# Kernel tuning notes

Hardware: AMD Instinct MI355X
Metric: run time of the kernel (lower is better)

Reference implementation:

```python
import jax, jax.numpy as jnp
import numpy as np

NUM_HEADS = 8
T = 8  # hardcoded temporal dim in the original forward
MD = 3  # max_displacement -> 7x7 window
EPS = 1e-12  # F.normalize eps


def l2_normalize(x, axis):
    n = jnp.sqrt(jnp.sum(x * x, axis=axis, keepdims=True))
    return x / jnp.maximum(n, EPS)


def correlation_7x7(q, k):
    # q, k: [B, C, H, W]; FlowNet-style correlation, kernel_size=1, max_disp=3.
    # out[b, u, v, h, w] = sum_c q[b,c,h,w] * k[b,c,h+u-3,w+v-3] (zero padded)
    B, C, H, W = q.shape
    kp = jnp.pad(k, ((0, 0), (0, 0), (MD, MD), (MD, MD)))
    outs = []
    for dy in range(2 * MD + 1):
        for dx in range(2 * MD + 1):
            ks = kp[:, :, dy:dy + H, dx:dx + W]
            outs.append(jnp.sum(q * ks, axis=1))  # [B, H, W]
    corr = jnp.stack(outs, axis=1)  # [B, 49, H, W]
    return corr.reshape(B, 2 * MD + 1, 2 * MD + 1, H, W)


def setup_inputs() -> dict:
    key = jax.random.key(0)
    ks = jax.random.split(key, 6)
    B, N, C = 8, 8192, 256
    hd = C // NUM_HEADS
    std = 0.02
    return {
        "x": jax.random.normal(ks[0], (B, N, C), dtype=jnp.float32),
        "w_qk": jax.random.normal(ks[1], (2 * C, C), dtype=jnp.float32) * std,
        "w_corr": jax.random.normal(ks[2], (hd, 49), dtype=jnp.float32) * std,
        "b_corr": jnp.zeros((hd,), dtype=jnp.float32),
        "w_proj": jax.random.normal(ks[3], (C, C), dtype=jnp.float32) * std,
        "b_proj": jnp.zeros((C,), dtype=jnp.float32),
    }


def reference(x, w_qk, w_corr, b_corr, w_proj, b_proj):
    B, N, C = x.shape
    nh = NUM_HEADS
    hd = C // nh
    H = int(np.sqrt(N // T))
    W = H

    # qk projection (no bias): [B, N, 2C] -> q, k each [B, nh, N, hd]
    qk = jnp.einsum('bnc,dc->bnd', x, w_qk)
    qk = qk.reshape(B, N, 2, nh, hd).transpose(2, 0, 3, 1, 4)
    q, k = qk[0], qk[1]

    # 'b n (t h w) d -> (b n) t d h w'
    q = q.reshape(B * nh, T, H, W, hd).transpose(0, 1, 4, 2, 3)
    k = k.reshape(B * nh, T, H, W, hd).transpose(0, 1, 4, 2, 3)

    # temporal postfix: k[t+1], last frame repeated
    k_post = jnp.concatenate([k[:, 1:], k[:, -1:]], axis=1)

    qp = q.reshape(B * nh * T, hd, H, W)
    kp = k_post.reshape(B * nh * T, hd, H, W)
    qp = l2_normalize(qp, axis=1)
    kp = l2_normalize(kp, axis=1)

    corr = correlation_7x7(qp, kp)  # [(B nh T), 7, 7, H, W]
    # 'b u v h w -> b (h w) (u v)'
    corr = corr.transpose(0, 3, 4, 1, 2).reshape(B * nh * T, H * W, 49)

    v = jnp.einsum('bpk,dk->bpd', corr, w_corr) + b_corr  # [(B nh T), HW, hd]

    # '(b n t) (h w) d -> b n (t h w) d' then 'b h n d -> b n (h d)'
    out = v.reshape(B, nh, T * H * W, hd).transpose(0, 2, 1, 3).reshape(B, N, C)
    out = jnp.einsum('bnc,dc->bnd', out, w_proj) + b_proj
    return out
```

## Files before the change

kernel.cpp:

```cpp
#include <hip/hip_runtime.h>

typedef _Float16 half8 __attribute__((ext_vector_type(8)));
typedef _Float16 half2v __attribute__((ext_vector_type(2)));
typedef float float4v __attribute__((ext_vector_type(4)));

__device__ __forceinline__ float dot2acc(unsigned a, unsigned b, float c) {
#if __has_builtin(__builtin_amdgcn_fdot2)
  return __builtin_amdgcn_fdot2(__builtin_bit_cast(half2v, a), __builtin_bit_cast(half2v, b), c, false);
#else
  half2v ha = __builtin_bit_cast(half2v, a);
  half2v hb = __builtin_bit_cast(half2v, b);
  c += (float)ha[0] * (float)hb[0];
  c += (float)ha[1] * (float)hb[1];
  return c;
#endif
}
__device__ __forceinline__ unsigned hscale(unsigned a, float s) {
  half2v ha = __builtin_bit_cast(half2v, a);
  half2v r;
  r[0] = (_Float16)((float)ha[0] * s);
  r[1] = (_Float16)((float)ha[1] * s);
  return __builtin_bit_cast(unsigned, r);
}
__device__ __forceinline__ void gload_lds16(const void* g, void* l) {
  __builtin_amdgcn_global_load_lds((const __attribute__((address_space(1))) unsigned*)g,
                                   (__attribute__((address_space(3))) unsigned*)l, 16, 0, 0);
}

__global__ void cvt_all(const float4* __restrict__ x, const float4* __restrict__ wqk,
                        const float4* __restrict__ wpj,
                        ushort4* __restrict__ x16, ushort4* __restrict__ wqk16,
                        ushort4* __restrict__ wpj16) {
  int b = blockIdx.x;
  const float4* s;
  ushort4* d;
  int i;
  if (b < 16384) { s = x; d = x16; i = b * 256 + threadIdx.x; }
  else if (b < 16512) { s = wqk; d = wqk16; i = (b - 16384) * 256 + threadIdx.x; }
  else { s = wpj; d = wpj16; i = (b - 16512) * 256 + threadIdx.x; }
  float4 v = s[i];
  _Float16 a = (_Float16)v.x, bb = (_Float16)v.y, c = (_Float16)v.z, e = (_Float16)v.w;
  ushort4 o;
  o.x = __builtin_bit_cast(unsigned short, a);
  o.y = __builtin_bit_cast(unsigned short, bb);
  o.z = __builtin_bit_cast(unsigned short, c);
  o.w = __builtin_bit_cast(unsigned short, e);
  d[i] = o;
}

__global__ __launch_bounds__(256, 2)
void gemm_qk(const _Float16* __restrict__ A, const _Float16* __restrict__ Bw,
             _Float16* __restrict__ qo, _Float16* __restrict__ ko) {
  __shared__ _Float16 Ash[4096];
  __shared__ _Float16 Bsh[4096];
  const int tid = threadIdx.x;
  const int lane = tid & 63, w = tid >> 6;
  const int wm = w >> 1, wn = w & 1;
  const int ml = lane & 15, qd = lane >> 4;
  const int m0 = blockIdx.y * 128, n0 = blockIdx.x * 128;

  float4v acc[4][4];
  float4v z = {0.f, 0.f, 0.f, 0.f};
#pragma unroll
  for (int i = 0; i < 4; ++i)
#pragma unroll
    for (int j = 0; j < 4; ++j) acc[i][j] = z;

  const _Float16* Ap = A + (size_t)m0 * 256;
  const _Float16* Bp = Bw + (size_t)n0 * 256;
  const int gr = w * 64 + lane;
  const int row0 = gr >> 2, kb = gr & 3;

  for (int kt = 0; kt < 8; ++kt) {
    int k0 = kt * 32;
    gload_lds16(Ap + row0 * 256 + k0 + kb * 8, Ash + (size_t)(w * 64) * 8);
    gload_lds16(Ap + (row0 + 64) * 256 + k0 + kb * 8, Ash + (size_t)(256 + w * 64) * 8);
    gload_lds16(Bp + row0 * 256 + k0 + kb * 8, Bsh + (size_t)(w * 64) * 8);
    gload_lds16(Bp + (row0 + 64) * 256 + k0 + kb * 8, Bsh + (size_t)(256 + w * 64) * 8);
    __syncthreads();
    half8 af[4], bf[4];
#pragma unroll
    for (int im = 0; im < 4; ++im) {
      af[im] = *(const half8*)(Ash + (wm * 64 + im * 16 + ml) * 32 + qd * 8);
      bf[im] = *(const half8*)(Bsh + (wn * 64 + im * 16 + ml) * 32 + qd * 8);
    }
#pragma unroll
    for (int im = 0; im < 4; ++im)
#pragma unroll
      for (int in = 0; in < 4; ++in)
        acc[im][in] = __builtin_amdgcn_mfma_f32_16x16x32_f16(af[im], bf[in], acc[im][in], 0, 0, 0);
    __syncthreads();
  }

#pragma unroll
  for (int im = 0; im < 4; ++im) {
    int rowr0 = m0 + wm * 64 + im * 16 + qd * 4;
#pragma unroll
    for (int in = 0; in < 4; ++in) {
      int col = n0 + wn * 64 + in * 16 + ml;
      int s = col >> 8, h = (col >> 5) & 7, j = col & 31;
      _Float16* dst = s ? ko : qo;
#pragma unroll
      for (int r = 0; r < 4; ++r) {
        int rowr = rowr0 + r;
        int b = rowr >> 13, n = rowr & 8191;
        int t = n >> 10, yx = n & 1023;
        int p = b * 64 + h * 8 + t;
        dst[((size_t)p * 1024 + yx) * 32 + j] = (_Float16)acc[im][in][r];
      }
    }
  }
}

__global__ __launch_bounds__(256, 4)
void corr_kernel(const _Float16* __restrict__ q16, const _Float16* __restrict__ k16,
                 const float* __restrict__ wcorr, const float* __restrict__ bcorr,
                 _Float16* __restrict__ outp) {
  __shared__ uint4 smem[2304];
  __shared__ uint4 wcs[256];

  const int tid = threadIdx.x;
  const int bx = blockIdx.x;
  const int p = bx >> 2, tile = bx & 3;
  const int y0 = (tile >> 1) * 16, x0 = (tile & 1) * 16;
  const int b = p >> 6, h = (p >> 3) & 7, t = p & 7;
  const int pk = (t < 7) ? p + 1 : p;
  const int ty = tid >> 4, tx = tid & 15;

  _Float16* wch = (_Float16*)wcs;
  for (int idx = tid; idx < 2048; idx += 256) {
    int d = idx >> 6, kk = idx & 63;
    float v = (kk < 49) ? wcorr[d * 49 + kk] : (kk == 49 ? bcorr[d] : 0.f);
    wch[idx] = (_Float16)v;
  }

  const _Float16* kbase = k16 + (size_t)pk * 32768;
#pragma unroll
  for (int i = 0; i < 8; ++i) {
    int g = tid + i * 256;
    if (g < 1936) {
      int vec = g >> 2, part = g & 3;
      int ky = vec / 22, kx = vec - ky * 22;
      int gy = y0 + ky - 3, gx = x0 + kx - 3;
      uint4 val = make_uint4(0u, 0u, 0u, 0u);
      if (gy >= 0 && gy < 32 && gx >= 0 && gx < 32)
        val = *(const uint4*)(kbase + ((size_t)gy * 32 + gx) * 32 + part * 8);
      int slot = (vec << 2) | (part ^ (vec & 3) ^ ((vec >> 2) & 3));
      smem[slot] = val;
    }
  }
  __syncthreads();

  for (int v = tid; v < 484; v += 256) {
    int base = v << 2;
    int sw = (v & 3) ^ ((v >> 2) & 3);
    uint4 gg[4];
#pragma unroll
    for (int pq = 0; pq < 4; ++pq) gg[pq] = smem[base | (pq ^ sw)];
    float ss = 0.f;
#pragma unroll
    for (int pq = 0; pq < 4; ++pq) {
      const unsigned* u = (const unsigned*)&gg[pq];
#pragma unroll
      for (int e = 0; e < 4; ++e) ss = dot2acc(u[e], u[e], ss);
    }
    float sc = 1.f / fmaxf(sqrtf(ss), 1e-12f);
#pragma unroll
    for (int pq = 0; pq < 4; ++pq) {
      unsigned* u = (unsigned*)&gg[pq];
#pragma unroll
      for (int e = 0; e < 4; ++e) u[e] = hscale(u[e], sc);
      smem[base | (pq ^ sw)] = gg[pq];
    }
  }
  __syncthreads();

  const _Float16* qptr = q16 + (size_t)p * 32768 + ((size_t)(y0 + ty) * 32 + (x0 + tx)) * 32;
  uint4 qv[4];
#pragma unroll
  for (int i = 0; i < 4; ++i) qv[i] = *(const uint4*)(qptr + i * 8);
  unsigned* qu = (unsigned*)qv;
  float qss = 0.f;
#pragma unroll
  for (int e = 0; e < 16; ++e) qss = dot2acc(qu[e], qu[e], qss);
  float qsc = 1.f / fmaxf(sqrtf(qss), 1e-12f);
#pragma unroll
  for (int e = 0; e < 16; ++e) qu[e] = hscale(qu[e], qsc);

  float corr[49];
#pragma unroll
  for (int dy = 0; dy < 7; ++dy) {
#pragma unroll
    for (int dx = 0; dx < 7; ++dx) {
      int vec = (ty + dy) * 22 + (tx + dx);
      int base = vec << 2;
      int sw = (vec & 3) ^ ((vec >> 2) & 3);
      float c = 0.f;
#pragma unroll
      for (int pq = 0; pq < 4; ++pq) {
        uint4 kk = smem[base | (pq ^ sw)];
        const unsigned* ku = (const unsigned*)&kk;
#pragma unroll
        for (int e = 0; e < 4; ++e) c = dot2acc(qu[pq * 4 + e], ku[e], c);
      }
      corr[dy * 7 + dx] = c;
    }
  }
  __syncthreads();

#pragma unroll
  for (int i = 0; i < 8; ++i) {
    uint4 val;
    unsigned* vu = (unsigned*)&val;
#pragma unroll
    for (int e = 0; e < 4; ++e) {
      int idx = i * 8 + e * 2;
      half2v hh;
      hh[0] = (_Float16)(idx < 49 ? corr[idx] : (idx == 49 ? 1.f : 0.f));
      hh[1] = (_Float16)(idx + 1 < 49 ? corr[idx + 1] : (idx + 1 == 49 ? 1.f : 0.f));
      vu[e] = __builtin_bit_cast(unsigned, hh);
    }
    smem[tid * 9 + i] = val;
  }
  __syncthreads();

  _Float16* corrm = (_Float16*)smem;
  const int lane = tid & 63, w = tid >> 6;
  const int ml = lane & 15, qd = lane >> 4;
  float4v vacc[4][2];
  float4v z = {0.f, 0.f, 0.f, 0.f};
#pragma unroll
  for (int im = 0; im < 4; ++im) { vacc[im][0] = z; vacc[im][1] = z; }
#pragma unroll
  for (int ks = 0; ks < 2; ++ks) {
    half8 bfrag[2];
#pragma unroll
    for (int nt = 0; nt < 2; ++nt)
      bfrag[nt] = *(const half8*)(wch + (nt * 16 + ml) * 64 + ks * 32 + qd * 8);
#pragma unroll
    for (int im = 0; im < 4; ++im) {
      half8 afrag = *(const half8*)(corrm + (w * 64 + im * 16 + ml) * 72 + ks * 32 + qd * 8);
#pragma unroll
      for (int nt = 0; nt < 2; ++nt)
        vacc[im][nt] = __builtin_amdgcn_mfma_f32_16x16x32_f16(afrag, bfrag[nt], vacc[im][nt], 0, 0, 0);
    }
  }

#pragma unroll
  for (int im = 0; im < 4; ++im) {
#pragma unroll
    for (int nt = 0; nt < 2; ++nt) {
      int d = nt * 16 + ml;
#pragma unroll
      for (int r = 0; r < 4; ++r) {
        int pos = w * 64 + im * 16 + qd * 4 + r;
        int py = pos >> 4, px = pos & 15;
        int n = t * 1024 + (y0 + py) * 32 + (x0 + px);
        outp[(((size_t)b * 8192 + n) << 8) + h * 32 + d] = (_Float16)vacc[im][nt][r];
      }
    }
  }
}

__global__ __launch_bounds__(256, 2)
void gemm_proj(const _Float16* __restrict__ A, const _Float16* __restrict__ Bw,
               const float* __restrict__ bp, float* __restrict__ out) {
  __shared__ _Float16 Ash[4096];
  __shared__ _Float16 Bsh[4096];
  const int tid = threadIdx.x;
  const int lane = tid & 63, w = tid >> 6;
  const int wm = w >> 1, wn = w & 1;
  const int ml = lane & 15, qd = lane >> 4;
  const int m0 = blockIdx.y * 128, n0 = blockIdx.x * 128;

  float4v acc[4][4];
  float4v z = {0.f, 0.f, 0.f, 0.f};
#pragma unroll
  for (int i = 0; i < 4; ++i)
#pragma unroll
    for (int j = 0; j < 4; ++j) acc[i][j] = z;

  const _Float16* Ap = A + (size_t)m0 * 256;
  const _Float16* Bp = Bw + (size_t)n0 * 256;
  const int gr = w * 64 + lane;
  const int row0 = gr >> 2, kb = gr & 3;

  for (int kt = 0; kt < 8; ++kt) {
    int k0 = kt * 32;
    gload_lds16(Ap + row0 * 256 + k0 + kb * 8, Ash + (size_t)(w * 64) * 8);
    gload_lds16(Ap + (row0 + 64) * 256 + k0 + kb * 8, Ash + (size_t)(256 + w * 64) * 8);
    gload_lds16(Bp + row0 * 256 + k0 + kb * 8, Bsh + (size_t)(w * 64) * 8);
    gload_lds16(Bp + (row0 + 64) * 256 + k0 + kb * 8, Bsh + (size_t)(256 + w * 64) * 8);
    __syncthreads();
    half8 af[4], bf[4];
#pragma unroll
    for (int im = 0; im < 4; ++im) {
      af[im] = *(const half8*)(Ash + (wm * 64 + im * 16 + ml) * 32 + qd * 8);
      bf[im] = *(const half8*)(Bsh + (wn * 64 + im * 16 + ml) * 32 + qd * 8);
    }
#pragma unroll
    for (int im = 0; im < 4; ++im)
#pragma unroll
      for (int in = 0; in < 4; ++in)
        acc[im][in] = __builtin_amdgcn_mfma_f32_16x16x32_f16(af[im], bf[in], acc[im][in], 0, 0, 0);
    __syncthreads();
  }

#pragma unroll
  for (int im = 0; im < 4; ++im) {
    int rowr0 = m0 + wm * 64 + im * 16 + qd * 4;
#pragma unroll
    for (int in = 0; in < 4; ++in) {
      int col = n0 + wn * 64 + in * 16 + ml;
      float bias = bp[col];
#pragma unroll
      for (int r = 0; r < 4; ++r)
        out[(size_t)(rowr0 + r) * 256 + col] = acc[im][in][r] + bias;
    }
  }
}

extern "C" void kernel_launch(void* const* d_in, const int* in_sizes, int n_in,
                              void* d_out, int out_size, void* d_ws, size_t ws_size,
                              hipStream_t stream) {
  const float* x      = (const float*)d_in[0];
  const float* w_qk   = (const float*)d_in[1];
  const float* w_corr = (const float*)d_in[2];
  const float* b_corr = (const float*)d_in[3];
  const float* w_proj = (const float*)d_in[4];
  const float* b_proj = (const float*)d_in[5];
  float* out = (float*)d_out;

  char* ws = (char*)d_ws;
  _Float16* x16   = (_Float16*)(ws);
  _Float16* q16   = (_Float16*)(ws + 33554432);
  _Float16* k16   = (_Float16*)(ws + 67108864);
  _Float16* op16  = (_Float16*)(ws + 100663296);
  _Float16* wqk16 = (_Float16*)(ws + 134217728);
  _Float16* wpj16 = (_Float16*)(ws + 134479872);

  cvt_all<<<16576, 256, 0, stream>>>((const float4*)x, (const float4*)w_qk, (const float4*)w_proj,
                                     (ushort4*)x16, (ushort4*)wqk16, (ushort4*)wpj16);
  gemm_qk<<<dim3(4, 512), 256, 0, stream>>>(x16, wqk16, q16, k16);
  corr_kernel<<<2048, 256, 0, stream>>>(q16, k16, w_corr, b_corr, op16);
  gemm_proj<<<dim3(2, 512), 256, 0, stream>>>(op16, wpj16, b_proj, out);
}
```

Baseline: 235.1 us.

## Compute 7x7 correlation with MFMA tiles instead of scalar dot2 loops

After: 244.1 us. 3.8% more time.

```diff
diff --git a/kernel.cpp b/kernel.cpp
--- a/kernel.cpp
+++ b/kernel.cpp
@@ -112,12 +112,15 @@
   }
 }
 
-__global__ __launch_bounds__(256, 4)
+__global__ __launch_bounds__(256, 2)
 void corr_kernel(const _Float16* __restrict__ q16, const _Float16* __restrict__ k16,
                  const float* __restrict__ wcorr, const float* __restrict__ bcorr,
                  _Float16* __restrict__ outp) {
-  __shared__ uint4 smem[2304];
-  __shared__ uint4 wcs[256];
+  __shared__ __align__(16) _Float16 S[38400];
+  _Float16* kt = S;
+  _Float16* corrh = S + 15488;
+  _Float16* wch = S + 35968;
+  constexpr int DUMP = 22528;
 
   const int tid = threadIdx.x;
   const int bx = blockIdx.x;
@@ -125,9 +128,18 @@
   const int y0 = (tile >> 1) * 16, x0 = (tile & 1) * 16;
   const int b = p >> 6, h = (p >> 3) & 7, t = p & 7;
   const int pk = (t < 7) ? p + 1 : p;
-  const int ty = tid >> 4, tx = tid & 15;
-
-  _Float16* wch = (_Float16*)wcs;
+
+  const int lane = tid & 63, w = tid >> 6;
+  const int ml = lane & 15, qd = lane >> 4;
+
+  const _Float16* qbase = q16 + (size_t)p * 32768;
+  half8 afrag[4];
+#pragma unroll
+  for (int yi = 0; yi < 4; ++yi) {
+    int yy = 4 * w + yi;
+    afrag[yi] = *(const half8*)(qbase + ((size_t)(y0 + yy) * 32 + (x0 + ml)) * 32 + qd * 8);
+  }
+
   for (int idx = tid; idx < 2048; idx += 256) {
     int d = idx >> 6, kk = idx & 63;
     float v = (kk < 49) ? wcorr[d * 49 + kk] : (kk == 49 ? bcorr[d] : 0.f);
@@ -145,90 +157,80 @@
       uint4 val = make_uint4(0u, 0u, 0u, 0u);
       if (gy >= 0 && gy < 32 && gx >= 0 && gx < 32)
         val = *(const uint4*)(kbase + ((size_t)gy * 32 + gx) * 32 + part * 8);
-      int slot = (vec << 2) | (part ^ (vec & 3) ^ ((vec >> 2) & 3));
-      smem[slot] = val;
-    }
-  }
+      *(uint4*)(kt + (size_t)g * 8) = val;
+    }
+  }
+
+#pragma unroll
+  for (int yi = 0; yi < 4; ++yi) {
+    unsigned* au = (unsigned*)&afrag[yi];
+    float ss = 0.f;
+#pragma unroll
+    for (int e = 0; e < 4; ++e) ss = dot2acc(au[e], au[e], ss);
+    ss += __shfl_xor(ss, 16);
+    ss += __shfl_xor(ss, 32);
+    float sc = 1.f / fmaxf(sqrtf(ss), 1e-12f);
+#pragma unroll
+    for (int e = 0; e < 4; ++e) au[e] = hscale(au[e], sc);
+  }
+
+  {
+    uint4 pat = make_uint4(0x3C000000u, 0u, 0u, 0u);
+    uint4 zz = make_uint4(0u, 0u, 0u, 0u);
+    *(uint4*)(corrh + (size_t)tid * 80 + 48) = pat;
+    *(uint4*)(corrh + (size_t)tid * 80 + 56) = zz;
+  }
+
   __syncthreads();
 
-  for (int v = tid; v < 484; v += 256) {
-    int base = v << 2;
-    int sw = (v & 3) ^ ((v >> 2) & 3);
-    uint4 gg[4];
-#pragma unroll
-    for (int pq = 0; pq < 4; ++pq) gg[pq] = smem[base | (pq ^ sw)];
-    float ss = 0.f;
-#pragma unroll
-    for (int pq = 0; pq < 4; ++pq) {
-      const unsigned* u = (const unsigned*)&gg[pq];
+#pragma unroll
+  for (int i = 0; i < 8; ++i) {
+    int g = tid + i * 256;
+    if (g < 1936) {
+      uint4 val = *(const uint4*)(kt + (size_t)g * 8);
+      unsigned* u = (unsigned*)&val;
+      float ss = 0.f;
 #pragma unroll
       for (int e = 0; e < 4; ++e) ss = dot2acc(u[e], u[e], ss);
-    }
-    float sc = 1.f / fmaxf(sqrtf(ss), 1e-12f);
-#pragma unroll
-    for (int pq = 0; pq < 4; ++pq) {
-      unsigned* u = (unsigned*)&gg[pq];
+      ss += __shfl_xor(ss, 1);
+      ss += __shfl_xor(ss, 2);
+      float sc = 1.f / fmaxf(sqrtf(ss), 1e-12f);
 #pragma unroll
       for (int e = 0; e < 4; ++e) u[e] = hscale(u[e], sc);
-      smem[base | (pq ^ sw)] = gg[pq];
+      *(uint4*)(kt + (size_t)g * 8) = val;
     }
   }
   __syncthreads();
 
-  const _Float16* qptr = q16 + (size_t)p * 32768 + ((size_t)(y0 + ty) * 32 + (x0 + tx)) * 32;
-  uint4 qv[4];
-#pragma unroll
-  for (int i = 0; i < 4; ++i) qv[i] = *(const uint4*)(qptr + i * 8);
-  unsigned* qu = (unsigned*)qv;
-  float qss = 0.f;
-#pragma unroll
-  for (int e = 0; e < 16; ++e) qss = dot2acc(qu[e], qu[e], qss);
-  float qsc = 1.f / fmaxf(sqrtf(qss), 1e-12f);
-#pragma unroll
-  for (int e = 0; e < 16; ++e) qu[e] = hscale(qu[e], qsc);
-
-  float corr[49];
-#pragma unroll
-  for (int dy = 0; dy < 7; ++dy) {
-#pragma unroll
-    for (int dx = 0; dx < 7; ++dx) {
-      int vec = (ty + dy) * 22 + (tx + dx);
-      int base = vec << 2;
-      int sw = (vec & 3) ^ ((vec >> 2) & 3);
-      float c = 0.f;
-#pragma unroll
-      for (int pq = 0; pq < 4; ++pq) {
-        uint4 kk = smem[base | (pq ^ sw)];
-        const unsigned* ku = (const unsigned*)&kk;
-#pragma unroll
-        for (int e = 0; e < 4; ++e) c = dot2acc(qu[pq * 4 + e], ku[e], c);
-      }
-      corr[dy * 7 + dx] = c;
+  const int bdx = ml - 4 * qd;
+  const int lanebase = 5120 * w + 320 * qd + bdx;
+  float4v z = {0.f, 0.f, 0.f, 0.f};
+#pragma unroll
+  for (int kri = 0; kri < 10; ++kri) {
+    int kr = 4 * w + kri;
+    half8 bf0 = *(const half8*)(kt + ((size_t)kr * 22 + ml) * 32 + qd * 8);
+    half8 bf1 = *(const half8*)(kt + ((size_t)kr * 22 + 16 + ml) * 32 + qd * 8);
+#pragma unroll
+    for (int yi = 0; yi < 4; ++yi) {
+      int dy = kri - yi;
+      if (dy < 0 || dy > 6) continue;
+      float4v r0 = __builtin_amdgcn_mfma_f32_16x16x32_f16(afrag[yi], bf0, z, 0, 0, 0);
+      float4v r1 = __builtin_amdgcn_mfma_f32_16x16x32_f16(afrag[yi], bf1, z, 0, 0, 0);
+#pragma unroll
+      for (int nt = 0; nt < 2; ++nt)
+#pragma unroll
+        for (int r = 0; r < 4; ++r) {
+          int dx = bdx + (16 * nt - r);
+          bool ok = (unsigned)dx <= 6u;
+          int idx = lanebase + (1280 * yi + 7 * dy + 79 * r + 16 * nt);
+          int off = ok ? idx : (DUMP + lane);
+          corrh[off] = (_Float16)((nt ? r1 : r0)[r]);
+        }
     }
   }
   __syncthreads();
 
-#pragma unroll
-  for (int i = 0; i < 8; ++i) {
-    uint4 val;
-    unsigned* vu = (unsigned*)&val;
-#pragma unroll
-    for (int e = 0; e < 4; ++e) {
-      int idx = i * 8 + e * 2;
-      half2v hh;
-      hh[0] = (_Float16)(idx < 49 ? corr[idx] : (idx == 49 ? 1.f : 0.f));
-      hh[1] = (_Float16)(idx + 1 < 49 ? corr[idx + 1] : (idx + 1 == 49 ? 1.f : 0.f));
-      vu[e] = __builtin_bit_cast(unsigned, hh);
-    }
-    smem[tid * 9 + i] = val;
-  }
-  __syncthreads();
-
-  _Float16* corrm = (_Float16*)smem;
-  const int lane = tid & 63, w = tid >> 6;
-  const int ml = lane & 15, qd = lane >> 4;
   float4v vacc[4][2];
-  float4v z = {0.f, 0.f, 0.f, 0.f};
 #pragma unroll
   for (int im = 0; im < 4; ++im) { vacc[im][0] = z; vacc[im][1] = z; }
 #pragma unroll
@@ -239,10 +241,10 @@
       bfrag[nt] = *(const half8*)(wch + (nt * 16 + ml) * 64 + ks * 32 + qd * 8);
 #pragma unroll
     for (int im = 0; im < 4; ++im) {
-      half8 afrag = *(const half8*)(corrm + (w * 64 + im * 16 + ml) * 72 + ks * 32 + qd * 8);
+      half8 afr = *(const half8*)(corrh + (size_t)(w * 64 + im * 16 + ml) * 80 + ks * 32 + qd * 8);
 #pragma unroll
       for (int nt = 0; nt < 2; ++nt)
-        vacc[im][nt] = __builtin_amdgcn_mfma_f32_16x16x32_f16(afrag, bfrag[nt], vacc[im][nt], 0, 0, 0);
+        vacc[im][nt] = __builtin_amdgcn_mfma_f32_16x16x32_f16(afr, bfrag[nt], vacc[im][nt], 0, 0, 0);
     }
   }
 
```

## Double-buffer LDS in GEMMs and swap MFMA operands for vectorized stores

Applied to the files above, without the earlier changes.

New measurement: 230.9 us. No clear change (-1.8%).

```diff
diff --git a/kernel.cpp b/kernel.cpp
--- a/kernel.cpp
+++ b/kernel.cpp
@@ -21,6 +21,12 @@
   r[0] = (_Float16)((float)ha[0] * s);
   r[1] = (_Float16)((float)ha[1] * s);
   return __builtin_bit_cast(unsigned, r);
+}
+__device__ __forceinline__ unsigned pack2(float a, float b) {
+  half2v h;
+  h[0] = (_Float16)a;
+  h[1] = (_Float16)b;
+  return __builtin_bit_cast(unsigned, h);
 }
 __device__ __forceinline__ void gload_lds16(const void* g, void* l) {
   __builtin_amdgcn_global_load_lds((const __attribute__((address_space(1))) unsigned*)g,
@@ -51,8 +57,8 @@
 __global__ __launch_bounds__(256, 2)
 void gemm_qk(const _Float16* __restrict__ A, const _Float16* __restrict__ Bw,
              _Float16* __restrict__ qo, _Float16* __restrict__ ko) {
-  __shared__ _Float16 Ash[4096];
-  __shared__ _Float16 Bsh[4096];
+  __shared__ _Float16 Ash[8192];
+  __shared__ _Float16 Bsh[8192];
   const int tid = threadIdx.x;
   const int lane = tid & 63, w = tid >> 6;
   const int wm = w >> 1, wn = w & 1;
@@ -71,43 +77,56 @@
   const int gr = w * 64 + lane;
   const int row0 = gr >> 2, kb = gr & 3;
 
+  {
+    gload_lds16(Ap + row0 * 256 + kb * 8, Ash + (size_t)(w * 64) * 8);
+    gload_lds16(Ap + (row0 + 64) * 256 + kb * 8, Ash + (size_t)(256 + w * 64) * 8);
+    gload_lds16(Bp + row0 * 256 + kb * 8, Bsh + (size_t)(w * 64) * 8);
+    gload_lds16(Bp + (row0 + 64) * 256 + kb * 8, Bsh + (size_t)(256 + w * 64) * 8);
+  }
+  __syncthreads();
+
+#pragma unroll
   for (int kt = 0; kt < 8; ++kt) {
-    int k0 = kt * 32;
-    gload_lds16(Ap + row0 * 256 + k0 + kb * 8, Ash + (size_t)(w * 64) * 8);
-    gload_lds16(Ap + (row0 + 64) * 256 + k0 + kb * 8, Ash + (size_t)(256 + w * 64) * 8);
-    gload_lds16(Bp + row0 * 256 + k0 + kb * 8, Bsh + (size_t)(w * 64) * 8);
-    gload_lds16(Bp + (row0 + 64) * 256 + k0 + kb * 8, Bsh + (size_t)(256 + w * 64) * 8);
+    const int cur = kt & 1;
+    if (kt < 7) {
+      const int k0 = (kt + 1) * 32;
+      const int nb = (cur ^ 1) * 4096;
+      gload_lds16(Ap + row0 * 256 + k0 + kb * 8, Ash + nb + (size_t)(w * 64) * 8);
+      gload_lds16(Ap + (row0 + 64) * 256 + k0 + kb * 8, Ash + nb + (size_t)(256 + w * 64) * 8);
+      gload_lds16(Bp + row0 * 256 + k0 + kb * 8, Bsh + nb + (size_t)(w * 64) * 8);
+      gload_lds16(Bp + (row0 + 64) * 256 + k0 + kb * 8, Bsh + nb + (size_t)(256 + w * 64) * 8);
+    }
+    const _Float16* Ac = Ash + cur * 4096;
+    const _Float16* Bc = Bsh + cur * 4096;
+    half8 af[4], bf[4];
+#pragma unroll
+    for (int im = 0; im < 4; ++im) {
+      af[im] = *(const half8*)(Ac + (wm * 64 + im * 16 + ml) * 32 + qd * 8);
+      bf[im] = *(const half8*)(Bc + (wn * 64 + im * 16 + ml) * 32 + qd * 8);
+    }
+#pragma unroll
+    for (int im = 0; im < 4; ++im)
+#pragma unroll
+      for (int in = 0; in < 4; ++in)
+        acc[im][in] = __builtin_amdgcn_mfma_f32_16x16x32_f16(bf[in], af[im], acc[im][in], 0, 0, 0);
     __syncthreads();
-    half8 af[4], bf[4];
-#pragma unroll
-    for (int im = 0; im < 4; ++im) {
-      af[im] = *(const half8*)(Ash + (wm * 64 + im * 16 + ml) * 32 + qd * 8);
-      bf[im] = *(const half8*)(Bsh + (wn * 64 + im * 16 + ml) * 32 + qd * 8);
-    }
-#pragma unroll
-    for (int im = 0; im < 4; ++im)
-#pragma unroll
-      for (int in = 0; in < 4; ++in)
-        acc[im][in] = __builtin_amdgcn_mfma_f32_16x16x32_f16(af[im], bf[in], acc[im][in], 0, 0, 0);
-    __syncthreads();
   }
 
 #pragma unroll
   for (int im = 0; im < 4; ++im) {
-    int rowr0 = m0 + wm * 64 + im * 16 + qd * 4;
+    int rowr = m0 + wm * 64 + im * 16 + ml;
+    int b = rowr >> 13, n = rowr & 8191;
+    int t = n >> 10, yx = n & 1023;
 #pragma unroll
     for (int in = 0; in < 4; ++in) {
-      int col = n0 + wn * 64 + in * 16 + ml;
+      int col = n0 + wn * 64 + in * 16 + qd * 4;
       int s = col >> 8, h = (col >> 5) & 7, j = col & 31;
       _Float16* dst = s ? ko : qo;
-#pragma unroll
-      for (int r = 0; r < 4; ++r) {
-        int rowr = rowr0 + r;
-        int b = rowr >> 13, n = rowr & 8191;
-        int t = n >> 10, yx = n & 1023;
-        int p = b * 64 + h * 8 + t;
-        dst[((size_t)p * 1024 + yx) * 32 + j] = (_Float16)acc[im][in][r];
-      }
+      int p = b * 64 + h * 8 + t;
+      uint2 pk;
+      pk.x = pack2(acc[im][in][0], acc[im][in][1]);
+      pk.y = pack2(acc[im][in][2], acc[im][in][3]);
+      *(uint2*)(dst + ((size_t)p * 1024 + yx) * 32 + j) = pk;
     }
   }
 }
@@ -265,8 +284,8 @@
 __global__ __launch_bounds__(256, 2)
 void gemm_proj(const _Float16* __restrict__ A, const _Float16* __restrict__ Bw,
                const float* __restrict__ bp, float* __restrict__ out) {
-  __shared__ _Float16 Ash[4096];
-  __shared__ _Float16 Bsh[4096];
+  __shared__ _Float16 Ash[8192];
+  __shared__ _Float16 Bsh[8192];
   const int tid = threadIdx.x;
   const int lane = tid & 63, w = tid >> 6;
   const int wm = w >> 1, wn = w & 1;
@@ -285,37 +304,54 @@
   const int gr = w * 64 + lane;
   const int row0 = gr >> 2, kb = gr & 3;
 
+  {
+    gload_lds16(Ap + row0 * 256 + kb * 8, Ash + (size_t)(w * 64) * 8);
+    gload_lds16(Ap + (row0 + 64) * 256 + kb * 8, Ash + (size_t)(256 + w * 64) * 8);
+    gload_lds16(Bp + row0 * 256 + kb * 8, Bsh + (size_t)(w * 64) * 8);
+    gload_lds16(Bp + (row0 + 64) * 256 + kb * 8, Bsh + (size_t)(256 + w * 64) * 8);
+  }
+  __syncthreads();
+
+#pragma unroll
   for (int kt = 0; kt < 8; ++kt) {
-    int k0 = kt * 32;
-    gload_lds16(Ap + row0 * 256 + k0 + kb * 8, Ash + (size_t)(w * 64) * 8);
-    gload_lds16(Ap + (row0 + 64) * 256 + k0 + kb * 8, Ash + (size_t)(256 + w * 64) * 8);
-    gload_lds16(Bp + row0 * 256 + k0 + kb * 8, Bsh + (size_t)(w * 64) * 8);
-    gload_lds16(Bp + (row0 + 64) * 256 + k0 + kb * 8, Bsh + (size_t)(256 + w * 64) * 8);
+    const int cur = kt & 1;
+    if (kt < 7) {
+      const int k0 = (kt + 1) * 32;
+      const int nb = (cur ^ 1) * 4096;
+      gload_lds16(Ap + row0 * 256 + k0 + kb * 8, Ash + nb + (size_t)(w * 64) * 8);
+      gload_lds16(Ap + (row0 + 64) * 256 + k0 + kb * 8, Ash + nb + (size_t)(256 + w * 64) * 8);
+      gload_lds16(Bp + row0 * 256 + k0 + kb * 8, Bsh + nb + (size_t)(w * 64) * 8);
+      gload_lds16(Bp + (row0 + 64) * 256 + k0 + kb * 8, Bsh + nb + (size_t)(256 + w * 64) * 8);
+    }
+    const _Float16* Ac = Ash + cur * 4096;
+    const _Float16* Bc = Bsh + cur * 4096;
+    half8 af[4], bf[4];
+#pragma unroll
+    for (int im = 0; im < 4; ++im) {
+      af[im] = *(const half8*)(Ac + (wm * 64 + im * 16 + ml) * 32 + qd * 8);
+      bf[im] = *(const half8*)(Bc + (wn * 64 + im * 16 + ml) * 32 + qd * 8);
+    }
+#pragma unroll
+    for (int im = 0; im < 4; ++im)
+#pragma unroll
+      for (int in = 0; in < 4; ++in)
+        acc[im][in] = __builtin_amdgcn_mfma_f32_16x16x32_f16(bf[in], af[im], acc[im][in], 0, 0, 0);
     __syncthreads();
-    half8 af[4], bf[4];
-#pragma unroll
-    for (int im = 0; im < 4; ++im) {
-      af[im] = *(const half8*)(Ash + (wm * 64 + im * 16 + ml) * 32 + qd * 8);
-      bf[im] = *(const half8*)(Bsh + (wn * 64 + im * 16 + ml) * 32 + qd * 8);
-    }
-#pragma unroll
-    for (int im = 0; im < 4; ++im)
-#pragma unroll
-      for (int in = 0; in < 4; ++in)
-        acc[im][in] = __builtin_amdgcn_mfma_f32_16x16x32_f16(af[im], bf[in], acc[im][in], 0, 0, 0);
-    __syncthreads();
   }
 
 #pragma unroll
   for (int im = 0; im < 4; ++im) {
-    int rowr0 = m0 + wm * 64 + im * 16 + qd * 4;
+    int rowr = m0 + wm * 64 + im * 16 + ml;
 #pragma unroll
     for (int in = 0; in < 4; ++in) {
-      int col = n0 + wn * 64 + in * 16 + ml;
-      float bias = bp[col];
-#pragma unroll
-      for (int r = 0; r < 4; ++r)
-        out[(size_t)(rowr0 + r) * 256 + col] = acc[im][in][r] + bias;
+      int col = n0 + wn * 64 + in * 16 + qd * 4;
+      float4 bb = *(const float4*)(bp + col);
+      float4 o;
+      o.x = acc[im][in][0] + bb.x;
+      o.y = acc[im][in][1] + bb.y;
+      o.z = acc[im][in][2] + bb.z;
+      o.w = acc[im][in][3] + bb.w;
+      *(float4*)(out + (size_t)rowr * 256 + col) = o;
     }
   }
 }
```
